# Optimization experiments

Measured on AMD Instinct MI355X. Metric: run time of the kernel, lower is better.

## Reference

```python
import jax, jax.numpy as jnp
import numpy as np

N = 100000
E = 1600000
IN_C, HID_C, OUT_C = 40, 64, 3


def _sage_params(key, f_in, f_out):
    k1, k2, k3 = jax.random.split(key, 3)
    s = 1.0 / np.sqrt(f_in)
    return (jax.random.uniform(k1, (f_in, f_out), jnp.float32, -s, s),  # W_neigh (lin_l)
            jax.random.uniform(k2, (f_in, f_out), jnp.float32, -s, s),  # W_root  (lin_r)
            jax.random.uniform(k3, (f_out,), jnp.float32, -s, s))       # bias


def setup_inputs() -> dict:
    key = jax.random.key(0)
    ks = jax.random.split(key, 8)
    x = jax.random.normal(ks[0], (N, IN_C), jnp.float32)
    edge_index = jax.random.randint(ks[1], (2, E), 0, N, jnp.int64)
    dims = [(IN_C, HID_C), (HID_C, HID_C), (HID_C, OUT_C),   # encoder
            (OUT_C, HID_C), (HID_C, HID_C), (HID_C, IN_C)]   # decoder
    names = ['enc1', 'enc2', 'enc3', 'dec1', 'dec2', 'dec3']
    out = {'x': x, 'edge_index': edge_index}
    for name, (fi, fo), k in zip(names, dims, ks[2:]):
        Wl, Wr, b = _sage_params(k, fi, fo)
        out[name + '_Wl'] = Wl
        out[name + '_Wr'] = Wr
        out[name + '_b'] = b
    return out


def _sage_conv(h, src, dst, inv_deg, Wl, Wr, b):
    # mean-aggregate neighbor features (messages src -> dst), then linear.
    msg_sum = jax.ops.segment_sum(h[src], dst, num_segments=N)  # [N, F_in]
    agg = msg_sum * inv_deg                                      # mean aggregation
    return agg @ Wl + h @ Wr + b


def reference(x, edge_index,
              enc1_Wl, enc1_Wr, enc1_b, enc2_Wl, enc2_Wr, enc2_b,
              enc3_Wl, enc3_Wr, enc3_b, dec1_Wl, dec1_Wr, dec1_b,
              dec2_Wl, dec2_Wr, dec2_b, dec3_Wl, dec3_Wr, dec3_b):
    src, dst = edge_index[0], edge_index[1]
    deg = jax.ops.segment_sum(jnp.ones((E,), jnp.float32), dst, num_segments=N)
    inv_deg = (1.0 / jnp.maximum(deg, 1.0))[:, None]
    # encoder
    h = jax.nn.relu(_sage_conv(x, src, dst, inv_deg, enc1_Wl, enc1_Wr, enc1_b))
    h = jax.nn.relu(_sage_conv(h, src, dst, inv_deg, enc2_Wl, enc2_Wr, enc2_b))
    z = _sage_conv(h, src, dst, inv_deg, enc3_Wl, enc3_Wr, enc3_b)
    # decoder
    h = jax.nn.relu(_sage_conv(z, src, dst, inv_deg, dec1_Wl, dec1_Wr, dec1_b))
    h = jax.nn.relu(_sage_conv(h, src, dst, inv_deg, dec2_Wl, dec2_Wr, dec2_b))
    x_rec = _sage_conv(h, src, dst, inv_deg, dec3_Wl, dec3_Wr, dec3_b)
    return (x_rec, z)
```

## Files before the change

### kernel.cpp

```cpp
#include <hip/hip_runtime.h>
#include <stdint.h>

#define NNODES 100000
#define NEDGES 1600000
#define NB 98

typedef unsigned short ushort_t;
typedef __attribute__((ext_vector_type(8))) short bf16x8;
typedef __attribute__((ext_vector_type(4))) float f32x4;

__device__ __forceinline__ float b2f(ushort_t u) {
  union { float f; uint32_t i; } v; v.i = ((uint32_t)u) << 16; return v.f;
}
__device__ __forceinline__ float blo(uint32_t p) {
  union { float f; uint32_t i; } v; v.i = p << 16; return v.f;
}
__device__ __forceinline__ float bhi(uint32_t p) {
  union { float f; uint32_t i; } v; v.i = p & 0xffff0000u; return v.f;
}
__device__ __forceinline__ ushort_t f2b(float f) {
  union { float f; uint32_t i; } v; v.f = f;
  uint32_t r = (v.i + 0x7fffu + ((v.i >> 16) & 1u)) >> 16;
  return (ushort_t)r;
}
__device__ __forceinline__ uint32_t pack2(float lo, float hi) {
  return (uint32_t)f2b(lo) | ((uint32_t)f2b(hi) << 16);
}
__device__ __forceinline__ int clampn(int i) {
  return i < 0 ? 0 : (i >= NNODES ? NNODES - 1 : i);
}

__global__ void detect_k(const uint32_t* __restrict__ x, const uint32_t* __restrict__ ei,
                         int* __restrict__ flags) {
  if (blockIdx.x == 0 && threadIdx.x == 0) {
    int cf = 0, ci = 0;
    for (int i = 0; i < 256; ++i) {
      uint32_t u = x[i];
      uint32_t e = (u >> 7) & 0xFFu;
      if (e >= 100u && e <= 141u) cf++;
      if (ei[2 * i + 1] == 0u) ci++;
    }
    flags[0] = (cf >= 128) ? 1 : 0;
    flags[1] = (ci >= 128) ? 1 : 0;
  }
}

__global__ void zero_i32(int* __restrict__ p, int n) {
  int i = blockIdx.x * blockDim.x + threadIdx.x;
  if (i < n) p[i] = 0;
}

__global__ void hist_k(const uint32_t* __restrict__ ei, int* __restrict__ deg,
                       const int* __restrict__ flags) {
  int e = blockIdx.x * blockDim.x + threadIdx.x;
  if (e >= NEDGES) return;
  int i64 = flags[1];
  int d = i64 ? (int)ei[2 * (size_t)NEDGES + 2 * (size_t)e] : (int)ei[(size_t)NEDGES + e];
  atomicAdd(&deg[clampn(d)], 1);
}

__global__ __launch_bounds__(1024) void scan1_k(const int* __restrict__ deg, int* __restrict__ bsum) {
  __shared__ int wsum[16];
  int tid = threadIdx.x;
  int i = blockIdx.x * 1024 + tid;
  int v = (i < NNODES) ? deg[i] : 0;
  #pragma unroll
  for (int d = 32; d >= 1; d >>= 1) v += __shfl_down(v, d);
  if ((tid & 63) == 0) wsum[tid >> 6] = v;
  __syncthreads();
  if (tid == 0) {
    int t = 0;
    #pragma unroll
    for (int w = 0; w < 16; ++w) t += wsum[w];
    bsum[blockIdx.x] = t;
  }
}

__global__ void scan2_k(int* __restrict__ bsum, int* __restrict__ offs) {
  if (blockIdx.x == 0 && threadIdx.x == 0) {
    int run = 0;
    for (int b = 0; b < NB; ++b) { int t = bsum[b]; bsum[b] = run; run += t; }
    offs[NNODES] = run;
  }
}

__global__ __launch_bounds__(1024) void scan3_k(const int* __restrict__ deg, const int* __restrict__ bsum,
                                                int* __restrict__ offs, int* __restrict__ cursor,
                                                float* __restrict__ invd) {
  __shared__ int wsum[16];
  int tid = threadIdx.x;
  int lane = tid & 63, wid = tid >> 6;
  int i = blockIdx.x * 1024 + tid;
  int v = (i < NNODES) ? deg[i] : 0;
  int s = v;
  #pragma unroll
  for (int d = 1; d < 64; d <<= 1) {
    int t = __shfl_up(s, d);
    if (lane >= d) s += t;
  }
  if (lane == 63) wsum[wid] = s;
  __syncthreads();
  int wprefix = 0;
  #pragma unroll
  for (int w = 0; w < 16; ++w)
    if (w < wid) wprefix += wsum[w];
  if (i < NNODES) {
    int excl = bsum[blockIdx.x] + wprefix + s - v;
    offs[i] = excl;
    cursor[i] = excl;
    invd[i] = 1.0f / fmaxf((float)v, 1.0f);
  }
}

__global__ void scatter4_k(const uint32_t* __restrict__ ei, int* __restrict__ cursor,
                           int* __restrict__ csr, const int* __restrict__ flags,
                           int lo, int hi) {
  int e = blockIdx.x * blockDim.x + threadIdx.x;
  if (e >= NEDGES) return;
  int i64 = flags[1];
  int s, d;
  if (i64) {
    d = (int)ei[2 * (size_t)NEDGES + 2 * (size_t)e];
    d = clampn(d);
    if (d < lo || d >= hi) return;
    s = (int)ei[2 * (size_t)e];
  } else {
    d = (int)ei[(size_t)NEDGES + e];
    d = clampn(d);
    if (d < lo || d >= hi) return;
    s = (int)ei[e];
  }
  int p = atomicAdd(&cursor[d], 1);
  if (p >= 0 && p < NEDGES) csr[p] = clampn(s);
}

template <bool BF16>
__global__ void cvt_packx_k(const void* __restrict__ src, uint32_t* __restrict__ dst, int npairs,
                            const int* __restrict__ flags) {
  if (flags[0] != (BF16 ? 1 : 0)) return;
  int i = blockIdx.x * blockDim.x + threadIdx.x;
  if (i < npairs) {
    if constexpr (BF16) dst[i] = ((const uint32_t*)src)[i];
    else {
      const float* s = (const float*)src;
      dst[i] = pack2(s[2 * i], s[2 * i + 1]);
    }
  }
}

template <bool BF16>
__global__ void cvt_outp_k(const uint32_t* __restrict__ src, void* __restrict__ dst, int npairs,
                           const int* __restrict__ flags) {
  if (flags[0] != (BF16 ? 1 : 0)) return;
  int i = blockIdx.x * blockDim.x + threadIdx.x;
  if (i < npairs) {
    if constexpr (BF16) ((uint32_t*)dst)[i] = src[i];
    else {
      uint32_t w = src[i];
      float* d = (float*)dst;
      d[2 * i] = blo(w);
      d[2 * i + 1] = bhi(w);
    }
  }
}

template <bool BF16>
__global__ void cvt_out_k(const float* __restrict__ src, void* __restrict__ dst, int n,
                          const int* __restrict__ flags) {
  if (flags[0] != (BF16 ? 1 : 0)) return;
  int i = blockIdx.x * blockDim.x + threadIdx.x;
  if (i < n) {
    if constexpr (BF16) ((ushort_t*)dst)[i] = f2b(src[i]);
    else ((float*)dst)[i] = src[i];
  }
}

struct WPtrs { const void* p[18]; int sz[18]; int off[18]; };

template <bool BF16>
__global__ void cvt_w_k(WPtrs w, float* __restrict__ dst, const int* __restrict__ flags) {
  if (flags[0] != (BF16 ? 1 : 0)) return;
  int a = blockIdx.x;
  int sz = w.sz[a], off = w.off[a];
  for (int t = threadIdx.x; t < sz; t += blockDim.x) {
    dst[off + t] = BF16 ? b2f(((const ushort_t*)w.p[a])[t]) : ((const float*)w.p[a])[t];
  }
}

template <bool ADD_U>
__global__ __launch_bounds__(256) void agg3_k(const float* __restrict__ feat, const int* __restrict__ csr,
                                              const int* __restrict__ offs, const float* __restrict__ invd,
                                              const float* __restrict__ u, float* __restrict__ out) {
  int n = blockIdx.x * blockDim.x + threadIdx.x;
  if (n >= NNODES) return;
  int k0 = offs[n], k1 = offs[n + 1];
  float a0 = 0.f, a1 = 0.f, a2 = 0.f;
  int k = k0;
  for (; k + 4 <= k1; k += 4) {
    const float* r0 = feat + (size_t)csr[k] * 3;
    const float* r1 = feat + (size_t)csr[k + 1] * 3;
    const float* r2 = feat + (size_t)csr[k + 2] * 3;
    const float* r3 = feat + (size_t)csr[k + 3] * 3;
    a0 += r0[0] + r1[0] + r2[0] + r3[0];
    a1 += r0[1] + r1[1] + r2[1] + r3[1];
    a2 += r0[2] + r1[2] + r2[2] + r3[2];
  }
  for (; k < k1; ++k) {
    const float* r = feat + (size_t)csr[k] * 3;
    a0 += r[0]; a1 += r[1]; a2 += r[2];
  }
  float iv = invd[n];
  a0 *= iv; a1 *= iv; a2 *= iv;
  if constexpr (ADD_U) {
    a0 += u[(size_t)n * 3];
    a1 += u[(size_t)n * 3 + 1];
    a2 += u[(size_t)n * 3 + 2];
  }
  out[(size_t)n * 3]     = a0;
  out[(size_t)n * 3 + 1] = a1;
  out[(size_t)n * 3 + 2] = a2;
}

template <int PAIRS, bool ADD_U>
__global__ __launch_bounds__(256) void aggp2_k(const uint32_t* __restrict__ feat, const int* __restrict__ csr,
                                               const int* __restrict__ offs, const float* __restrict__ invd,
                                               const uint32_t* __restrict__ u, uint32_t* __restrict__ out) {
  int lane = threadIdx.x & 63;
  int n = (blockIdx.x * blockDim.x + threadIdx.x) >> 6;
  if (n >= NNODES) return;
  int half = lane >> 5;
  int p = lane & 31;
  int k0 = offs[n], k1 = offs[n + 1];
  float aL = 0.f, aH = 0.f;
  int k = k0;
  for (; k + 8 <= k1; k += 8) {
    int i0 = csr[k + half], i1 = csr[k + 2 + half], i2 = csr[k + 4 + half], i3 = csr[k + 6 + half];
    if (p < PAIRS) {
      uint32_t w0 = feat[(size_t)i0 * PAIRS + p];
      uint32_t w1 = feat[(size_t)i1 * PAIRS + p];
      uint32_t w2 = feat[(size_t)i2 * PAIRS + p];
      uint32_t w3 = feat[(size_t)i3 * PAIRS + p];
      aL += blo(w0) + blo(w1) + blo(w2) + blo(w3);
      aH += bhi(w0) + bhi(w1) + bhi(w2) + bhi(w3);
    }
  }
  for (; k < k1; k += 2) {
    int kk = k + half;
    if (kk < k1 && p < PAIRS) {
      uint32_t w = feat[(size_t)csr[kk] * PAIRS + p];
      aL += blo(w);
      aH += bhi(w);
    }
  }
  aL += __shfl_xor(aL, 32);
  aH += __shfl_xor(aH, 32);
  if (half == 0 && p < PAIRS) {
    float iv = invd[n];
    float vL = aL * iv, vH = aH * iv;
    if constexpr (ADD_U) {
      uint32_t uw = u[(size_t)n * PAIRS + p];
      vL += blo(uw);
      vH += bhi(uw);
    }
    out[(size_t)n * PAIRS + p] = pack2(vL, vH);
  }
}

template <int F_IN, int F_OUT, bool DUAL, bool RELU, bool PIN, bool POUT>
__global__ __launch_bounds__(256) void mgemm_k(const void* __restrict__ Av, const void* __restrict__ Bv,
                                               const float* __restrict__ W1, const float* __restrict__ W2,
                                               const float* __restrict__ Wb,
                                               void* __restrict__ C1v, void* __restrict__ C2v) {
  constexpr int KS = (F_IN + 31) / 32;
  constexpr int JT = (F_OUT + 15) / 16;
  constexpr int PP = F_IN / 2;
  int lane = threadIdx.x & 63;
  int wid  = threadIdx.x >> 6;
  int tile = blockIdx.x * 4 + wid;
  if (tile * 16 >= NNODES) return;
  int l15 = lane & 15, l4 = lane >> 4;

  bf16x8 w1f[KS][JT], w2f[KS][JT];
  float bv[JT];
  #pragma unroll
  for (int ks = 0; ks < KS; ++ks) {
    #pragma unroll
    for (int jt = 0; jt < JT; ++jt) {
      int col = jt * 16 + l15;
      #pragma unroll
      for (int j = 0; j < 8; ++j) {
        int k = ks * 32 + l4 * 8 + j;
        bool ok = (k < F_IN) && (col < F_OUT);
        w1f[ks][jt][j] = ok ? (short)f2b(W1[k * F_OUT + col]) : (short)0;
        w2f[ks][jt][j] = ok ? (short)f2b(W2[k * F_OUT + col]) : (short)0;
      }
    }
  }
  #pragma unroll
  for (int jt = 0; jt < JT; ++jt) {
    int col = jt * 16 + l15;
    bv[jt] = (col < F_OUT) ? Wb[col] : 0.f;
  }

  int row = tile * 16 + l15;
  bf16x8 af[KS], bfr[KS];
  if constexpr (PIN) {
    const uint32_t* Arow = (const uint32_t*)Av + (size_t)row * PP;
    #pragma unroll
    for (int ks = 0; ks < KS; ++ks) {
      #pragma unroll
      for (int w4 = 0; w4 < 4; ++w4) {
        int word = ks * 16 + l4 * 4 + w4;
        uint32_t v = (word < PP) ? Arow[word] : 0u;
        af[ks][2 * w4]     = (short)(v & 0xffffu);
        af[ks][2 * w4 + 1] = (short)(v >> 16);
      }
    }
    if constexpr (!DUAL) {
      const uint32_t* Brow = (const uint32_t*)Bv + (size_t)row * PP;
      #pragma unroll
      for (int ks = 0; ks < KS; ++ks) {
        #pragma unroll
        for (int w4 = 0; w4 < 4; ++w4) {
          int word = ks * 16 + l4 * 4 + w4;
          uint32_t v = (word < PP) ? Brow[word] : 0u;
          bfr[ks][2 * w4]     = (short)(v & 0xffffu);
          bfr[ks][2 * w4 + 1] = (short)(v >> 16);
        }
      }
    }
  } else {
    const float* Arow = (const float*)Av + (size_t)row * F_IN;
    #pragma unroll
    for (int ks = 0; ks < KS; ++ks) {
      #pragma unroll
      for (int j = 0; j < 8; ++j) {
        int k = ks * 32 + l4 * 8 + j;
        af[ks][j] = (k < F_IN) ? (short)f2b(Arow[k]) : (short)0;
      }
    }
    if constexpr (!DUAL) {
      const float* Brow = (const float*)Bv + (size_t)row * F_IN;
      #pragma unroll
      for (int ks = 0; ks < KS; ++ks) {
        #pragma unroll
        for (int j = 0; j < 8; ++j) {
          int k = ks * 32 + l4 * 8 + j;
          bfr[ks][j] = (k < F_IN) ? (short)f2b(Brow[k]) : (short)0;
        }
      }
    }
  }

  f32x4 acc1[JT], acc2[DUAL ? JT : 1];
  #pragma unroll
  for (int jt = 0; jt < JT; ++jt) {
    acc1[jt] = (f32x4)(0.f);
    if constexpr (DUAL) acc2[jt] = (f32x4)(0.f);
  }

  #pragma unroll
  for (int ks = 0; ks < KS; ++ks) {
    #pragma unroll
    for (int jt = 0; jt < JT; ++jt) {
      acc1[jt] = __builtin_amdgcn_mfma_f32_16x16x32_bf16(af[ks], w1f[ks][jt], acc1[jt], 0, 0, 0);
      if constexpr (DUAL)
        acc2[jt] = __builtin_amdgcn_mfma_f32_16x16x32_bf16(af[ks], w2f[ks][jt], acc2[jt], 0, 0, 0);
      else
        acc1[jt] = __builtin_amdgcn_mfma_f32_16x16x32_bf16(bfr[ks], w2f[ks][jt], acc1[jt], 0, 0, 0);
    }
  }

  #pragma unroll
  for (int jt = 0; jt < JT; ++jt) {
    int col = jt * 16 + l15;
    #pragma unroll
    for (int r = 0; r < 4; ++r) {
      int orow = tile * 16 + l4 * 4 + r;
      if constexpr (DUAL) {
        float v1 = acc1[jt][r];
        float v2 = acc2[jt][r] + bv[jt];
        if constexpr (POUT) {
          float p1 = __shfl_xor(v1, 1);
          float p2 = __shfl_xor(v2, 1);
          if (((lane & 1) == 0) && col < F_OUT) {
            ((uint32_t*)C1v)[(size_t)orow * (F_OUT / 2) + (col >> 1)] = pack2(v1, p1);
            ((uint32_t*)C2v)[(size_t)orow * (F_OUT / 2) + (col >> 1)] = pack2(v2, p2);
          }
        } else {
          if (col < F_OUT) {
            ((float*)C1v)[(size_t)orow * F_OUT + col] = v1;
            ((float*)C2v)[(size_t)orow * F_OUT + col] = v2;
          }
        }
      } else {
        float v = acc1[jt][r] + bv[jt];
        if constexpr (RELU) v = fmaxf(v, 0.f);
        if constexpr (POUT) {
          float pv = __shfl_xor(v, 1);
          if (((lane & 1) == 0) && col < F_OUT)
            ((uint32_t*)C1v)[(size_t)orow * (F_OUT / 2) + (col >> 1)] = pack2(v, pv);
        } else {
          if (col < F_OUT)
            ((float*)C1v)[(size_t)orow * F_OUT + col] = v;
        }
      }
    }
  }
}

extern "C" void kernel_launch(void* const* d_in, const int* in_sizes, int n_in,
                              void* d_out, int out_size, void* d_ws, size_t ws_size,
                              hipStream_t stream) {
  const uint32_t* xw = (const uint32_t*)d_in[0];
  const uint32_t* ei = (const uint32_t*)d_in[1];

  char* ws = (char*)d_ws;
  size_t off = 0;
  auto carve = [&](size_t bytes) -> char* {
    char* p = ws + off;
    off = (off + bytes + 255) & ~(size_t)255;
    return p;
  };
  int* flags     = (int*)carve(8);
  int* deg       = (int*)carve((size_t)NNODES * 4);
  int* offs      = (int*)carve((size_t)(NNODES + 1) * 4);
  int* cursor    = (int*)carve((size_t)NNODES * 4);
  float* invd    = (float*)carve((size_t)NNODES * 4);
  int* bsum      = (int*)carve((size_t)NB * 4);
  int* csr       = (int*)carve((size_t)NEDGES * 4);
  float* wf      = (float*)carve((size_t)32768 * 4);
  uint32_t* xp   = (uint32_t*)carve((size_t)NNODES * 20 * 4);
  uint32_t* mp   = (uint32_t*)carve((size_t)NNODES * 20 * 4);
  uint32_t* b0p  = (uint32_t*)carve((size_t)NNODES * 32 * 4);
  uint32_t* b1p  = (uint32_t*)carve((size_t)NNODES * 32 * 4);
  uint32_t* b2p  = (uint32_t*)carve((size_t)NNODES * 32 * 4);
  uint32_t* y40p = (uint32_t*)carve((size_t)NNODES * 20 * 4);
  uint32_t* u40p = (uint32_t*)carve((size_t)NNODES * 20 * 4);
  uint32_t* xrp  = (uint32_t*)carve((size_t)NNODES * 20 * 4);
  float* y3f     = (float*)carve((size_t)NNODES * 3 * 4);
  float* u3f     = (float*)carve((size_t)NNODES * 3 * 4);
  float* zf      = (float*)carve((size_t)NNODES * 3 * 4);
  float* m3f     = (float*)carve((size_t)NNODES * 3 * 4);

  static const int wsz[18] = {2560, 2560, 64, 4096, 4096, 64, 192, 192, 3,
                              192, 192, 64, 4096, 4096, 64, 2560, 2560, 40};
  WPtrs wp;
  int woff = 0;
  for (int i = 0; i < 18; ++i) {
    wp.p[i] = d_in[2 + i];
    wp.sz[i] = wsz[i];
    wp.off[i] = woff;
    woff += wsz[i];
  }
  const float* W[18];
  for (int i = 0; i < 18; ++i) W[i] = wf + wp.off[i];

  detect_k<<<1, 64, 0, stream>>>(xw, ei, flags);
  zero_i32<<<(NNODES + 255) / 256, 256, 0, stream>>>(deg, NNODES);
  hist_k<<<(NEDGES + 255) / 256, 256, 0, stream>>>(ei, deg, flags);
  scan1_k<<<NB, 1024, 0, stream>>>(deg, bsum);
  scan2_k<<<1, 64, 0, stream>>>(bsum, offs);
  scan3_k<<<NB, 1024, 0, stream>>>(deg, bsum, offs, cursor, invd);
  const int EB = (NEDGES + 255) / 256;
  scatter4_k<<<EB, 256, 0, stream>>>(ei, cursor, csr, flags, 0, 25000);
  scatter4_k<<<EB, 256, 0, stream>>>(ei, cursor, csr, flags, 25000, 50000);
  scatter4_k<<<EB, 256, 0, stream>>>(ei, cursor, csr, flags, 50000, 75000);
  scatter4_k<<<EB, 256, 0, stream>>>(ei, cursor, csr, flags, 75000, 100000);

  const int NXP = NNODES * 20;
  cvt_packx_k<false><<<(NXP + 255) / 256, 256, 0, stream>>>(d_in[0], xp, NXP, flags);
  cvt_packx_k<true ><<<(NXP + 255) / 256, 256, 0, stream>>>(d_in[0], xp, NXP, flags);
  cvt_w_k<false><<<18, 256, 0, stream>>>(wp, wf, flags);
  cvt_w_k<true ><<<18, 256, 0, stream>>>(wp, wf, flags);

  const int AGGW_BLOCKS = (NNODES * 64 + 255) / 256;
  const int AGG3_BLOCKS = (NNODES + 255) / 256;
  const int MG = (NNODES / 16 + 3) / 4;

  aggp2_k<20, false><<<AGGW_BLOCKS, 256, 0, stream>>>(xp, csr, offs, invd, nullptr, mp);
  mgemm_k<40, 64, false, true, true, true><<<MG, 256, 0, stream>>>(mp, xp, W[0], W[1], W[2], b1p, nullptr);
  aggp2_k<32, false><<<AGGW_BLOCKS, 256, 0, stream>>>(b1p, csr, offs, invd, nullptr, b0p);
  mgemm_k<64, 64, false, true, true, true><<<MG, 256, 0, stream>>>(b0p, b1p, W[3], W[4], W[5], b2p, nullptr);
  mgemm_k<64, 3, true, false, true, false><<<MG, 256, 0, stream>>>(b2p, nullptr, W[6], W[7], W[8], y3f, u3f);
  agg3_k<true><<<AGG3_BLOCKS, 256, 0, stream>>>(y3f, csr, offs, invd, u3f, zf);
  agg3_k<false><<<AGG3_BLOCKS, 256, 0, stream>>>(zf, csr, offs, invd, nullptr, m3f);
  mgemm_k<3, 64, false, true, false, true><<<MG, 256, 0, stream>>>(m3f, zf, W[9], W[10], W[11], b1p, nullptr);
  aggp2_k<32, false><<<AGGW_BLOCKS, 256, 0, stream>>>(b1p, csr, offs, invd, nullptr, b0p);
  mgemm_k<64, 64, false, true, true, true><<<MG, 256, 0, stream>>>(b0p, b1p, W[12], W[13], W[14], b2p, nullptr);
  mgemm_k<64, 40, true, false, true, true><<<MG, 256, 0, stream>>>(b2p, nullptr, W[15], W[16], W[17], y40p, u40p);
  aggp2_k<20, true><<<AGGW_BLOCKS, 256, 0, stream>>>(y40p, csr, offs, invd, u40p, xrp);

  const int NX = NNODES * 40;
  const int NZ = NNODES * 3;
  cvt_outp_k<false><<<(NXP + 255) / 256, 256, 0, stream>>>(xrp, d_out, NXP, flags);
  cvt_outp_k<true ><<<(NXP + 255) / 256, 256, 0, stream>>>(xrp, d_out, NXP, flags);
  cvt_out_k<false><<<(NZ + 255) / 256, 256, 0, stream>>>(zf, (float*)d_out + NX, NZ, flags);
  cvt_out_k<true ><<<(NZ + 255) / 256, 256, 0, stream>>>(zf, (ushort_t*)d_out + NX, NZ, flags);
  (void)in_sizes; (void)n_in; (void)out_size; (void)ws_size;
}
```

Baseline: 572.9 us.

## Build CSR with LDS-windowed histogram and per-slice cursors instead of global atomics

Replaces the global-atomic degree histogram and the four-pass global-atomic scatter with windowed shared-memory histograms. Each of 128 blocks handles one 25000-node window and one 50000-edge slice, writing per-slice counts that a reduce kernel turns into per-slice prefix offsets. The scatter then uses LDS cursors seeded from those offsets, so global atomic contention on deg and cursor goes away. In exchange only 128 blocks run, each reading its whole edge slice, and the csr buffer is zero-filled and aggregation indices are clamped for safety.

Result: slower. 595.0 us (+3.9%).

```diff
diff --git a/kernel.cpp b/kernel.cpp
--- a/kernel.cpp
+++ b/kernel.cpp
@@ -4,6 +4,9 @@
 #define NNODES 100000
 #define NEDGES 1600000
 #define NB 98
+#define WIN 25000
+#define NSL 32
+#define SLICE 50000
 
 typedef unsigned short ushort_t;
 typedef __attribute__((ext_vector_type(8))) short bf16x8;
@@ -50,13 +53,40 @@
   if (i < n) p[i] = 0;
 }
 
-__global__ void hist_k(const uint32_t* __restrict__ ei, int* __restrict__ deg,
-                       const int* __restrict__ flags) {
-  int e = blockIdx.x * blockDim.x + threadIdx.x;
-  if (e >= NEDGES) return;
+__global__ __launch_bounds__(256) void histw_k(const uint32_t* __restrict__ ei,
+                                               int* __restrict__ degp,
+                                               const int* __restrict__ flags) {
+  __shared__ int h[WIN];
+  int b = blockIdx.x;
+  int w = b >> 5, s = b & 31;
+  for (int j = threadIdx.x; j < WIN; j += 256) h[j] = 0;
+  __syncthreads();
   int i64 = flags[1];
-  int d = i64 ? (int)ei[2 * (size_t)NEDGES + 2 * (size_t)e] : (int)ei[(size_t)NEDGES + e];
-  atomicAdd(&deg[clampn(d)], 1);
+  int base = w * WIN;
+  int e0 = s * SLICE, e1 = e0 + SLICE;
+  for (int e = e0 + threadIdx.x; e < e1; e += 256) {
+    int d = i64 ? (int)ei[2 * (size_t)NEDGES + 2 * (size_t)e] : (int)ei[(size_t)NEDGES + e];
+    d = clampn(d);
+    int j = d - base;
+    if ((unsigned)j < (unsigned)WIN) atomicAdd(&h[j], 1);
+  }
+  __syncthreads();
+  int* dp = degp + (size_t)s * NNODES + base;
+  for (int j = threadIdx.x; j < WIN; j += 256) dp[j] = h[j];
+}
+
+__global__ void hreduce_k(int* __restrict__ degp, int* __restrict__ deg) {
+  int n = blockIdx.x * blockDim.x + threadIdx.x;
+  if (n >= NNODES) return;
+  int run = 0;
+  #pragma unroll
+  for (int s = 0; s < NSL; ++s) {
+    size_t idx = (size_t)s * NNODES + n;
+    int t = degp[idx];
+    degp[idx] = run;
+    run += t;
+  }
+  deg[n] = run;
 }
 
 __global__ __launch_bounds__(1024) void scan1_k(const int* __restrict__ deg, int* __restrict__ bsum) {
@@ -112,26 +142,30 @@
   }
 }
 
-__global__ void scatter4_k(const uint32_t* __restrict__ ei, int* __restrict__ cursor,
-                           int* __restrict__ csr, const int* __restrict__ flags,
-                           int lo, int hi) {
-  int e = blockIdx.x * blockDim.x + threadIdx.x;
-  if (e >= NEDGES) return;
+__global__ __launch_bounds__(256) void scatters_k(const uint32_t* __restrict__ ei,
+                                                  const int* __restrict__ offs,
+                                                  const int* __restrict__ degp,
+                                                  int* __restrict__ csr,
+                                                  const int* __restrict__ flags) {
+  __shared__ int cur[WIN];
+  int b = blockIdx.x;
+  int w = b >> 5, s = b & 31;
+  int base = w * WIN;
+  const int* dp = degp + (size_t)s * NNODES + base;
+  for (int j = threadIdx.x; j < WIN; j += 256) cur[j] = offs[base + j] + dp[j];
+  __syncthreads();
   int i64 = flags[1];
-  int s, d;
-  if (i64) {
-    d = (int)ei[2 * (size_t)NEDGES + 2 * (size_t)e];
+  int e0 = s * SLICE, e1 = e0 + SLICE;
+  for (int e = e0 + threadIdx.x; e < e1; e += 256) {
+    int d = i64 ? (int)ei[2 * (size_t)NEDGES + 2 * (size_t)e] : (int)ei[(size_t)NEDGES + e];
     d = clampn(d);
-    if (d < lo || d >= hi) return;
-    s = (int)ei[2 * (size_t)e];
-  } else {
-    d = (int)ei[(size_t)NEDGES + e];
-    d = clampn(d);
-    if (d < lo || d >= hi) return;
-    s = (int)ei[e];
-  }
-  int p = atomicAdd(&cursor[d], 1);
-  if (p >= 0 && p < NEDGES) csr[p] = clampn(s);
+    int j = d - base;
+    if ((unsigned)j < (unsigned)WIN) {
+      int src = i64 ? (int)ei[2 * (size_t)e] : (int)ei[e];
+      int p = atomicAdd(&cur[j], 1);
+      if (p >= 0 && p < NEDGES) csr[p] = clampn(src);
+    }
+  }
 }
 
 template <bool BF16>
@@ -197,16 +231,16 @@
   float a0 = 0.f, a1 = 0.f, a2 = 0.f;
   int k = k0;
   for (; k + 4 <= k1; k += 4) {
-    const float* r0 = feat + (size_t)csr[k] * 3;
-    const float* r1 = feat + (size_t)csr[k + 1] * 3;
-    const float* r2 = feat + (size_t)csr[k + 2] * 3;
-    const float* r3 = feat + (size_t)csr[k + 3] * 3;
+    const float* r0 = feat + (size_t)clampn(csr[k]) * 3;
+    const float* r1 = feat + (size_t)clampn(csr[k + 1]) * 3;
+    const float* r2 = feat + (size_t)clampn(csr[k + 2]) * 3;
+    const float* r3 = feat + (size_t)clampn(csr[k + 3]) * 3;
     a0 += r0[0] + r1[0] + r2[0] + r3[0];
     a1 += r0[1] + r1[1] + r2[1] + r3[1];
     a2 += r0[2] + r1[2] + r2[2] + r3[2];
   }
   for (; k < k1; ++k) {
-    const float* r = feat + (size_t)csr[k] * 3;
+    const float* r = feat + (size_t)clampn(csr[k]) * 3;
     a0 += r[0]; a1 += r[1]; a2 += r[2];
   }
   float iv = invd[n];
@@ -234,7 +268,8 @@
   float aL = 0.f, aH = 0.f;
   int k = k0;
   for (; k + 8 <= k1; k += 8) {
-    int i0 = csr[k + half], i1 = csr[k + 2 + half], i2 = csr[k + 4 + half], i3 = csr[k + 6 + half];
+    int i0 = clampn(csr[k + half]), i1 = clampn(csr[k + 2 + half]);
+    int i2 = clampn(csr[k + 4 + half]), i3 = clampn(csr[k + 6 + half]);
     if (p < PAIRS) {
       uint32_t w0 = feat[(size_t)i0 * PAIRS + p];
       uint32_t w1 = feat[(size_t)i1 * PAIRS + p];
@@ -247,7 +282,7 @@
   for (; k < k1; k += 2) {
     int kk = k + half;
     if (kk < k1 && p < PAIRS) {
-      uint32_t w = feat[(size_t)csr[kk] * PAIRS + p];
+      uint32_t w = feat[(size_t)clampn(csr[kk]) * PAIRS + p];
       aL += blo(w);
       aH += bhi(w);
     }
@@ -443,6 +478,8 @@
   float* zf      = (float*)carve((size_t)NNODES * 3 * 4);
   float* m3f     = (float*)carve((size_t)NNODES * 3 * 4);
 
+  int* degp = (int*)b0p;
+
   static const int wsz[18] = {2560, 2560, 64, 4096, 4096, 64, 192, 192, 3,
                               192, 192, 64, 4096, 4096, 64, 2560, 2560, 40};
   WPtrs wp;
@@ -457,16 +494,13 @@
   for (int i = 0; i < 18; ++i) W[i] = wf + wp.off[i];
 
   detect_k<<<1, 64, 0, stream>>>(xw, ei, flags);
-  zero_i32<<<(NNODES + 255) / 256, 256, 0, stream>>>(deg, NNODES);
-  hist_k<<<(NEDGES + 255) / 256, 256, 0, stream>>>(ei, deg, flags);
+  zero_i32<<<(NEDGES + 255) / 256, 256, 0, stream>>>(csr, NEDGES);
+  histw_k<<<128, 256, 0, stream>>>(ei, degp, flags);
+  hreduce_k<<<(NNODES + 255) / 256, 256, 0, stream>>>(degp, deg);
   scan1_k<<<NB, 1024, 0, stream>>>(deg, bsum);
   scan2_k<<<1, 64, 0, stream>>>(bsum, offs);
   scan3_k<<<NB, 1024, 0, stream>>>(deg, bsum, offs, cursor, invd);
-  const int EB = (NEDGES + 255) / 256;
-  scatter4_k<<<EB, 256, 0, stream>>>(ei, cursor, csr, flags, 0, 25000);
-  scatter4_k<<<EB, 256, 0, stream>>>(ei, cursor, csr, flags, 25000, 50000);
-  scatter4_k<<<EB, 256, 0, stream>>>(ei, cursor, csr, flags, 50000, 75000);
-  scatter4_k<<<EB, 256, 0, stream>>>(ei, cursor, csr, flags, 75000, 100000);
+  scatters_k<<<128, 256, 0, stream>>>(ei, offs, degp, csr, flags);
 
   const int NXP = NNODES * 20;
   cvt_packx_k<false><<<(NXP + 255) / 256, 256, 0, stream>>>(d_in[0], xp, NXP, flags);
```
